# Kernel optimization log

Hardware: AMD Instinct MI355X
Metric: run time of the kernel (lower is better)

Reference implementation:

```python
import jax, jax.numpy as jnp
import numpy as np

B, S, D, H = 4, 2048, 1024, 16
HD = D // H
EPS = 1e-5

def _ln(x, g, b):
    mu = jnp.mean(x, axis=-1, keepdims=True)
    var = jnp.mean(jnp.square(x - mu), axis=-1, keepdims=True)
    return (x - mu) * jax.lax.rsqrt(var + EPS) * g + b

def setup_inputs() -> dict:
    key = jax.random.key(0)
    ks = jax.random.split(key, 6)
    W = 0.02  # GPT-2 style init scale keeps softmax unsaturated
    causal = jnp.tril(jnp.ones((S, S), dtype=bool))
    mask = jnp.where(causal, 0.0, -1e9).astype(jnp.float32)[None, None]
    return {
        "x": jax.random.normal(ks[0], (B, S, D), jnp.float32),
        "attention_mask": mask,
        "ln1_g": jnp.ones((D,), jnp.float32),
        "ln1_b": jnp.zeros((D,), jnp.float32),
        "w_qkv": jax.random.normal(ks[1], (D, 3 * D), jnp.float32) * W,
        "b_qkv": jnp.zeros((3 * D,), jnp.float32),
        "w_ao": jax.random.normal(ks[2], (D, D), jnp.float32) * W,
        "b_ao": jnp.zeros((D,), jnp.float32),
        "ln2_g": jnp.ones((D,), jnp.float32),
        "ln2_b": jnp.zeros((D,), jnp.float32),
        "w_fc": jax.random.normal(ks[3], (D, 4 * D), jnp.float32) * W,
        "b_fc": jnp.zeros((4 * D,), jnp.float32),
        "w_out": jax.random.normal(ks[4], (4 * D, D), jnp.float32) * W,
        "b_out": jnp.zeros((D,), jnp.float32),
    }

def reference(x, attention_mask, ln1_g, ln1_b, w_qkv, b_qkv, w_ao, b_ao,
              ln2_g, ln2_b, w_fc, b_fc, w_out, b_out):
    b, s, d = x.shape
    h = _ln(x, ln1_g, ln1_b)
    qkv = h @ w_qkv + b_qkv  # [B,S,3D]
    q, k, v = jnp.split(qkv, 3, axis=-1)
    def heads(t):  # [B,S,D] -> [B,H,S,HD]
        return t.reshape(b, s, H, HD).transpose(0, 2, 1, 3)
    q, k, v = heads(q), heads(k), heads(v)
    att = jnp.einsum('bhqd,bhkd->bhqk', q, k) / jnp.sqrt(jnp.float32(HD))
    att = att + attention_mask
    att = jax.nn.softmax(att, axis=-1)
    out = jnp.einsum('bhqk,bhkd->bhqd', att, v)
    out = out.transpose(0, 2, 1, 3).reshape(b, s, d)
    x = x + out @ w_ao + b_ao
    h2 = _ln(x, ln2_g, ln2_b)
    # torch nn.GELU() default is exact erf gelu
    mlp = jax.nn.gelu(h2 @ w_fc + b_fc, approximate=False) @ w_out + b_out
    return x + mlp
```

## Files before the change

kernel.cpp:

```cpp
#include <hip/hip_runtime.h>

typedef unsigned short u16;
typedef __attribute__((ext_vector_type(8))) short short8;
typedef __attribute__((ext_vector_type(4))) float floatx4;
typedef __attribute__((ext_vector_type(4))) unsigned short ushort4_t;

#define S_LEN 2048
#define DMODEL 1024
#define NHEAD 16
#define HDIM 64

__device__ __forceinline__ u16 f2bf(float f) {
    union { float f; unsigned u; } v; v.f = f;
    unsigned u = v.u;
    unsigned r = (u + 0x7fffu + ((u >> 16) & 1u)) >> 16;
    return (u16)r;
}

__device__ __forceinline__ u16 f2bf_fast(float f) {
    union { float f; unsigned u; } v; v.f = f;
    return (u16)((v.u + 0x8000u) >> 16);
}

__device__ __forceinline__ void gld_lds16(const u16* g, u16* l) {
    __builtin_amdgcn_global_load_lds((const __attribute__((address_space(1))) void*)g,
                                     (__attribute__((address_space(3))) void*)l,
                                     16, 0, 0);
}

__global__ __launch_bounds__(256) void ln_kernel(
    const float* __restrict__ x, const float* __restrict__ g,
    const float* __restrict__ b, u16* __restrict__ out)
{
    int row = blockIdx.x;
    int tid = threadIdx.x;
    const float4* xr = (const float4*)(x + (size_t)row * DMODEL);
    float4 v = xr[tid];
    float s  = v.x + v.y + v.z + v.w;
    float s2 = v.x * v.x + v.y * v.y + v.z * v.z + v.w * v.w;
    #pragma unroll
    for (int off = 1; off < 64; off <<= 1) {
        s  += __shfl_xor(s, off, 64);
        s2 += __shfl_xor(s2, off, 64);
    }
    __shared__ float red[2][4];
    int w = tid >> 6, lane = tid & 63;
    if (lane == 0) { red[0][w] = s; red[1][w] = s2; }
    __syncthreads();
    s  = red[0][0] + red[0][1] + red[0][2] + red[0][3];
    s2 = red[1][0] + red[1][1] + red[1][2] + red[1][3];
    float mu  = s * (1.0f / DMODEL);
    float var = s2 * (1.0f / DMODEL) - mu * mu;
    float inv = rsqrtf(var + 1e-5f);
    const float4* gr = (const float4*)g;
    const float4* br = (const float4*)b;
    float4 gv = gr[tid], bv = br[tid];
    u16* o = out + (size_t)row * DMODEL + tid * 4;
    o[0] = f2bf((v.x - mu) * inv * gv.x + bv.x);
    o[1] = f2bf((v.y - mu) * inv * gv.y + bv.y);
    o[2] = f2bf((v.z - mu) * inv * gv.z + bv.z);
    o[3] = f2bf((v.w - mu) * inv * gv.w + bv.w);
}

__global__ __launch_bounds__(256) void prep_kernel(
    const float* __restrict__ x, const float* __restrict__ g,
    const float* __restrict__ b, u16* __restrict__ out,
    const float* __restrict__ w0, u16* __restrict__ d0,
    const float* __restrict__ w1, u16* __restrict__ d1,
    const float* __restrict__ w2, u16* __restrict__ d2,
    const float* __restrict__ w3, u16* __restrict__ d3)
{
    int id = blockIdx.x;
    int tid = threadIdx.x;
    if (id < 8192) {
        int row = id;
        const float4* xr = (const float4*)(x + (size_t)row * DMODEL);
        float4 v = xr[tid];
        float s  = v.x + v.y + v.z + v.w;
        float s2 = v.x * v.x + v.y * v.y + v.z * v.z + v.w * v.w;
        #pragma unroll
        for (int off = 1; off < 64; off <<= 1) {
            s  += __shfl_xor(s, off, 64);
            s2 += __shfl_xor(s2, off, 64);
        }
        __shared__ float red[2][4];
        int w = tid >> 6, lane = tid & 63;
        if (lane == 0) { red[0][w] = s; red[1][w] = s2; }
        __syncthreads();
        s  = red[0][0] + red[0][1] + red[0][2] + red[0][3];
        s2 = red[1][0] + red[1][1] + red[1][2] + red[1][3];
        float mu  = s * (1.0f / DMODEL);
        float var = s2 * (1.0f / DMODEL) - mu * mu;
        float inv = rsqrtf(var + 1e-5f);
        const float4* gr = (const float4*)g;
        const float4* br = (const float4*)b;
        float4 gv = gr[tid], bv = br[tid];
        u16* o = out + (size_t)row * DMODEL + tid * 4;
        o[0] = f2bf((v.x - mu) * inv * gv.x + bv.x);
        o[1] = f2bf((v.y - mu) * inv * gv.y + bv.y);
        o[2] = f2bf((v.z - mu) * inv * gv.z + bv.z);
        o[3] = f2bf((v.w - mu) * inv * gv.w + bv.w);
        return;
    }
    id -= 8192;
    __shared__ float t[32][33];
    const float* w; u16* wt; int K, N, bx, by;
    if (id < 3072)      { w = w0; wt = d0; K = 1024; N = 3072; bx = id % 96;  by = id / 96;  }
    else if (id < 4096) { id -= 3072; w = w1; wt = d1; K = 1024; N = 1024; bx = id & 31;  by = id >> 5; }
    else if (id < 8192) { id -= 4096; w = w2; wt = d2; K = 1024; N = 4096; bx = id & 127; by = id >> 7; }
    else                { id -= 8192; w = w3; wt = d3; K = 4096; N = 1024; bx = id & 31;  by = id >> 5; }
    int n0 = bx * 32, k0 = by * 32;
    int xx = tid & 31, yy = tid >> 5;
    #pragma unroll
    for (int j = yy; j < 32; j += 8)
        t[j][xx] = w[(size_t)(k0 + j) * N + n0 + xx];
    __syncthreads();
    #pragma unroll
    for (int j = yy; j < 32; j += 8)
        wt[(size_t)(n0 + j) * K + k0 + xx] = f2bf(t[xx][j]);
}

template<int MODE>
__global__ __launch_bounds__(256) void gemm_bt(
    const u16* __restrict__ A, const u16* __restrict__ BT,
    int M, int N, int K,
    const float* __restrict__ bias, const float* __restrict__ res,
    float* __restrict__ fout,
    u16* __restrict__ o0, u16* __restrict__ o1, u16* __restrict__ o2)
{
    __shared__ __attribute__((aligned(16))) u16 As[2][128 * 64];
    __shared__ __attribute__((aligned(16))) u16 Bs[2][128 * 64];
    int tid = threadIdx.x;
    int lane = tid & 63, w = tid >> 6;
    int wm = (w >> 1) * 64, wn = (w & 1) * 64;
    int l15 = lane & 15, quad = lane >> 4;
    int rowBase = blockIdx.y * 128, colBase = blockIdx.x * 128;

    floatx4 acc[4][4] = {};

    const u16* pa[4];
    const u16* pbt[4];
    int scb[4];
    #pragma unroll
    for (int i = 0; i < 4; ++i) {
        int c  = i * 256 + tid;
        int r  = c >> 3;
        int cs = ((c & 7) ^ (r & 7)) * 8;
        pa[i]  = A  + (size_t)(rowBase + r) * K + cs;
        pbt[i] = BT + (size_t)(colBase + r) * K + cs;
        scb[i] = (i * 256 + (tid & 0xC0)) * 8;
    }

    int KT = K >> 6;

    #pragma unroll
    for (int i = 0; i < 4; ++i) {
        gld_lds16(pa[i],  &As[0][0] + scb[i]);
        gld_lds16(pbt[i], &Bs[0][0] + scb[i]);
    }

    for (int kt = 0; kt < KT; ++kt) {
        __syncthreads();

        if (kt + 1 < KT) {
            u16* abuf = &As[(kt + 1) & 1][0];
            u16* bbuf = &Bs[(kt + 1) & 1][0];
            #pragma unroll
            for (int i = 0; i < 4; ++i) {
                pa[i]  += 64;
                pbt[i] += 64;
                gld_lds16(pa[i],  abuf + scb[i]);
                gld_lds16(pbt[i], bbuf + scb[i]);
            }
        }

        const u16* as = &As[kt & 1][0];
        const u16* bs = &Bs[kt & 1][0];
        #pragma unroll
        for (int ks = 0; ks < 2; ++ks) {
            int sw = (((ks * 4 + quad) ^ (l15 & 7))) * 8;
            short8 af[4], bf[4];
            #pragma unroll
            for (int im = 0; im < 4; ++im)
                af[im] = *(const short8*)(as + (wm + im * 16 + l15) * 64 + sw);
            #pragma unroll
            for (int in = 0; in < 4; ++in)
                bf[in] = *(const short8*)(bs + (wn + in * 16 + l15) * 64 + sw);
            #pragma unroll
            for (int im = 0; im < 4; ++im)
                #pragma unroll
                for (int in = 0; in < 4; ++in)
                    acc[im][in] = __builtin_amdgcn_mfma_f32_16x16x32_bf16(af[im], bf[in], acc[im][in], 0, 0, 0);
        }
    }

    if (MODE == 0) {
        int t = colBase >> 10;
        int cb1023 = colBase & 1023;
        if (t == 2) {
            #pragma unroll
            for (int im = 0; im < 4; ++im) {
                int gr0 = rowBase + wm + im * 16 + quad * 4;
                int bb2 = gr0 >> 11, ss = gr0 & 2047;
                #pragma unroll
                for (int in = 0; in < 4; ++in) {
                    int gc = colBase + wn + in * 16 + l15;
                    int rr = cb1023 + wn + in * 16 + l15;
                    int hh = rr >> 6, hd = rr & 63;
                    float bv = bias[gc];
                    ushort4_t pk;
                    pk.x = f2bf_fast(acc[im][in][0] + bv);
                    pk.y = f2bf_fast(acc[im][in][1] + bv);
                    pk.z = f2bf_fast(acc[im][in][2] + bv);
                    pk.w = f2bf_fast(acc[im][in][3] + bv);
                    *(ushort4_t*)(o1 + ((size_t)(bb2 * NHEAD + hh) * HDIM + hd) * S_LEN + ss) = pk;
                }
            }
        } else {
            u16* qb = o0 + (size_t)t * 8388608;
            float sc = (t == 0) ? 0.125f : 1.0f;
            #pragma unroll
            for (int im = 0; im < 4; ++im) {
                #pragma unroll
                for (int in = 0; in < 4; ++in) {
                    #pragma unroll
                    for (int r = 0; r < 4; ++r) {
                        int gr = rowBase + wm + im * 16 + quad * 4 + r;
                        int gc = colBase + wn + in * 16 + l15;
                        float v = (acc[im][in][r] + bias[gc]) * sc;
                        int rr = cb1023 + wn + in * 16 + l15;
                        int hh = rr >> 6, hd = rr & 63;
                        int bb2 = gr >> 11, ss = gr & 2047;
                        qb[(((size_t)(bb2 * NHEAD + hh) * S_LEN + ss) * HDIM) + hd] = f2bf_fast(v);
                    }
                }
            }
        }
    } else {
        #pragma unroll
        for (int im = 0; im < 4; ++im) {
            #pragma unroll
            for (int in = 0; in < 4; ++in) {
                #pragma unroll
                for (int r = 0; r < 4; ++r) {
                    int gr = rowBase + wm + im * 16 + quad * 4 + r;
                    int gc = colBase + wn + in * 16 + l15;
                    float v = acc[im][in][r] + bias[gc];
                    if (MODE == 2) {
                        float p = v * (1.59576912f + 0.07135481f * v * v);
                        float e = __expf(-p);
                        float gl = v * __builtin_amdgcn_rcpf(1.0f + e);
                        o0[(size_t)gr * N + gc] = f2bf_fast(gl);
                    } else {
                        fout[(size_t)gr * N + gc] = v + res[(size_t)gr * N + gc];
                    }
                }
            }
        }
    }
}

template<int MODE>
__global__ __launch_bounds__(512, 2) void gemm256(
    const u16* __restrict__ A, const u16* __restrict__ BT,
    int M, int N, int K,
    const float* __restrict__ bias,
    u16* __restrict__ o0, u16* __restrict__ o1)
{
    __shared__ __attribute__((aligned(16))) u16 As[2][2][128 * 64];
    __shared__ __attribute__((aligned(16))) u16 Bs[2][2][128 * 64];
    int tid = threadIdx.x;
    int lane = tid & 63, w = tid >> 6;
    int wrow = w >> 2, wcol = w & 3;
    int l15 = lane & 15, quad = lane >> 4;
    int rowBase = blockIdx.y * 256, colBase = blockIdx.x * 256;
    int nrb = (wcol & 1) * 64;

    int swz[2] = { (quad ^ (l15 & 7)) * 8, ((4 + quad) ^ (l15 & 7)) * 8 };

    int cid0 = tid, cid1 = 512 + tid;
    int r0 = cid0 >> 3, r1 = cid1 >> 3;
    unsigned cs0 = (unsigned)(((cid0 & 7) ^ (r0 & 7)) * 8);
    unsigned cs1 = (unsigned)(((cid1 & 7) ^ (r1 & 7)) * 8);
    unsigned aoff0 = (unsigned)((rowBase + r0) * K) + cs0;
    unsigned aoff1 = (unsigned)((rowBase + r1) * K) + cs1;
    unsigned boff0 = (unsigned)((colBase + r0) * K) + cs0;
    unsigned boff1 = (unsigned)((colBase + r1) * K) + cs1;
    unsigned ldo0 = (unsigned)(cid0 * 8), ldo1 = (unsigned)(cid1 * 8);
    unsigned hK = (unsigned)(128 * K);

    floatx4 acc[8][4] = {};
    short8 af[4][2], bfL[2][2], bfH[2][2];

    int KT = K >> 6;

#define STG_A(db, tt, h) do { unsigned tb_ = (unsigned)(tt) * 64u + (h) * hK;      \
    gld_lds16(A + aoff0 + tb_, &As[db][h][0] + ldo0);                              \
    gld_lds16(A + aoff1 + tb_, &As[db][h][0] + ldo1); } while (0)
#define STG_B(db, tt, h) do { unsigned tb_ = (unsigned)(tt) * 64u + (h) * hK;      \
    gld_lds16(BT + boff0 + tb_, &Bs[db][h][0] + ldo0);                             \
    gld_lds16(BT + boff1 + tb_, &Bs[db][h][0] + ldo1); } while (0)
#define LDS_A(buf, MFB) do { const u16* ap_ = &As[buf][wrow][0];                   \
    _Pragma("unroll") for (int m_ = 0; m_ < 4; ++m_) {                             \
      af[m_][0] = *(const short8*)(ap_ + (((MFB) + m_) * 16 + l15) * 64 + swz[0]); \
      af[m_][1] = *(const short8*)(ap_ + (((MFB) + m_) * 16 + l15) * 64 + swz[1]); } } while (0)
#define LDS_B(buf, NFP, dst) do { const u16* bp_ = &Bs[buf][wcol >> 1][0];         \
    _Pragma("unroll") for (int n_ = 0; n_ < 2; ++n_) {                             \
      dst[n_][0] = *(const short8*)(bp_ + (nrb + ((NFP) * 2 + n_) * 16 + l15) * 64 + swz[0]); \
      dst[n_][1] = *(const short8*)(bp_ + (nrb + ((NFP) * 2 + n_) * 16 + l15) * 64 + swz[1]); } } while (0)
#define MFMA_Q(MFB, NFP, bsrc) do { __builtin_amdgcn_s_setprio(1);                 \
    _Pragma("unroll") for (int m_ = 0; m_ < 4; ++m_)                               \
    _Pragma("unroll") for (int n_ = 0; n_ < 2; ++n_) {                             \
      acc[(MFB) + m_][(NFP) * 2 + n_] = __builtin_amdgcn_mfma_f32_16x16x32_bf16(af[m_][0], bsrc[n_][0], acc[(MFB) + m_][(NFP) * 2 + n_], 0, 0, 0); \
      acc[(MFB) + m_][(NFP) * 2 + n_] = __builtin_amdgcn_mfma_f32_16x16x32_bf16(af[m_][1], bsrc[n_][1], acc[(MFB) + m_][(NFP) * 2 + n_], 0, 0, 0); } \
    __builtin_amdgcn_s_setprio(0); } while (0)
#define PH_MID() do { __builtin_amdgcn_sched_barrier(0);                           \
    __builtin_amdgcn_s_barrier();                                                  \
    asm volatile("s_waitcnt lgkmcnt(0)" ::: "memory");                             \
    __builtin_amdgcn_sched_barrier(0); } while (0)
#define PH_END() do { __builtin_amdgcn_sched_barrier(0);                           \
    __builtin_amdgcn_s_barrier(); } while (0)

    STG_A(0, 0, 0); STG_A(0, 0, 1);
    STG_B(0, 0, 0); STG_B(0, 0, 1);
    STG_B(1, 1, 0); STG_B(1, 1, 1);
    STG_A(1, 1, 0);
    asm volatile("s_waitcnt vmcnt(6)" ::: "memory");
    __builtin_amdgcn_s_barrier();

    for (int t = 0; t < KT; t += 2) {
        int t2 = (t + 2 < KT) ? t + 2 : KT - 1;
        int t3 = (t + 3 < KT) ? t + 3 : KT - 1;

        LDS_A(0, 0); LDS_B(0, 0, bfL);
        STG_A(1, t + 1, 1);
        asm volatile("s_waitcnt lgkmcnt(8)" ::: "memory");
        PH_MID(); MFMA_Q(0, 0, bfL); PH_END();

        LDS_B(0, 1, bfH);
        PH_MID(); MFMA_Q(0, 1, bfH); PH_END();

        LDS_A(0, 4);
        STG_B(0, t2, 0);
        PH_MID(); MFMA_Q(4, 1, bfH); PH_END();

        STG_B(0, t2, 1);
        STG_A(0, t2, 0);
        asm volatile("s_waitcnt vmcnt(6)" ::: "memory");
        PH_MID(); MFMA_Q(4, 0, bfL); PH_END();

        LDS_A(1, 0); LDS_B(1, 0, bfL);
        STG_A(0, t2, 1);
        asm volatile("s_waitcnt lgkmcnt(8)" ::: "memory");
        PH_MID(); MFMA_Q(0, 0, bfL); PH_END();

        LDS_B(1, 1, bfH);
        PH_MID(); MFMA_Q(0, 1, bfH); PH_END();

        LDS_A(1, 4);
        STG_B(1, t3, 0);
        PH_MID(); MFMA_Q(4, 1, bfH); PH_END();

        STG_B(1, t3, 1);
        STG_A(1, t3, 0);
        asm volatile("s_waitcnt vmcnt(6)" ::: "memory");
        PH_MID(); MFMA_Q(4, 0, bfL); PH_END();
    }
    asm volatile("s_waitcnt vmcnt(0)" ::: "memory");

#undef STG_A
#undef STG_B
#undef LDS_A
#undef LDS_B
#undef MFMA_Q
#undef PH_MID
#undef PH_END

    int wr0 = rowBase + wrow * 128 + quad * 4;
    int wc0 = colBase + wcol * 64 + l15;
    #pragma unroll
    for (int mf = 0; mf < 8; ++mf) {
        #pragma unroll
        for (int nf = 0; nf < 4; ++nf) {
            int gc = wc0 + nf * 16;
            float bv = bias[gc];
            #pragma unroll
            for (int r = 0; r < 4; ++r) {
                int gr = wr0 + mf * 16 + r;
                float v = acc[mf][nf][r] + bv;
                float p = v * (1.59576912f + 0.07135481f * v * v);
                float e = __expf(-p);
                float gl = v * __builtin_amdgcn_rcpf(1.0f + e);
                o0[(size_t)gr * N + gc] = f2bf_fast(gl);
            }
        }
    }
}

__global__ __launch_bounds__(256) void flash_attn(
    const u16* __restrict__ Q, const u16* __restrict__ Kb,
    const u16* __restrict__ Vt, u16* __restrict__ O)
{
    __shared__ __attribute__((aligned(16))) u16 Ks[2][64 * 64];
    __shared__ __attribute__((aligned(16))) u16 Vs[2][64 * 64];
    __shared__ __attribute__((aligned(16))) u16 Pl[4][2][16][64];
    int tid = threadIdx.x;
    int lane = tid & 63, w = tid >> 6;
    int l15 = lane & 15, quad = lane >> 4;
    int bh = blockIdx.x;
    int pp = blockIdx.y;
    int bb = bh >> 4, h = bh & 15;

    const u16* Kp0 = Kb + (size_t)bh * S_LEN * HDIM;
    const u16* Vp  = Vt + (size_t)bh * HDIM * S_LEN;

    int rstage = lane >> 3;
    int cstage = ((lane & 7) ^ rstage) * 8;
    int vrow0  = w * 8 + rstage;

    int ms[2] = {pp, 15 - pp};
    int pb = 0;

    #pragma unroll
    for (int i = 0; i < 2; ++i) {
        int row = i * 32 + vrow0;
        gld_lds16(Kp0 + row * HDIM + cstage, &Ks[0][0] + i * 2048 + w * 512);
        gld_lds16(Vp + (size_t)row * S_LEN + cstage, &Vs[0][0] + i * 2048 + w * 512);
    }

    #pragma unroll 1
    for (int sel = 0; sel < 2; ++sel) {
        int m = ms[sel];
        int q0 = m * 128;

        const u16* Qp = Q + ((size_t)bh * S_LEN + q0 + w * 16) * HDIM;
        short8 aq0[2], aq1[2];
        #pragma unroll
        for (int ks = 0; ks < 2; ++ks) {
            aq0[ks] = *(const short8*)(Qp + l15 * HDIM + ks * 32 + quad * 8);
            aq1[ks] = *(const short8*)(Qp + 64 * HDIM + l15 * HDIM + ks * 32 + quad * 8);
        }

        floatx4 acc_o0[4] = {}, acc_o1[4] = {};
        float rs0 = 0.f, rs1 = 0.f;

        int KT = 2 * m + 2;

        auto softmax_store = [&](floatx4 (&sa)[4], float& rs, int st, bool diag) {
            #pragma unroll
            for (int nt = 0; nt < 4; ++nt) {
                ushort4_t pk;
                #pragma unroll
                for (int r = 0; r < 4; ++r) {
                    float sv = sa[nt][r];
                    if (diag) {
                        int kc = nt * 16 + quad * 4 + r;
                        if (kc > w * 16 + l15) sv = -1e30f;
                    }
                    float pv = __expf(sv);
                    rs += pv;
                    pk[r] = f2bf_fast(pv);
                }
                int chSw = (nt * 4 + quad) ^ (l15 & 14);
                *(ushort4_t*)(&Pl[w][st][l15][chSw * 4]) = pk;
            }
        };

        #pragma unroll 1
        for (int kt = 0; kt < KT; ++kt) {
            __syncthreads();
            int cur = pb;

            int nk = (kt + 1 < KT) ? (kt + 1) : ((sel < 1) ? 0 : -1);
            if (nk >= 0) {
                pb ^= 1;
                const u16* Kg = Kp0 + (size_t)nk * 64 * HDIM;
                const u16* Vg = Vp + nk * 64;
                u16* kb_ = &Ks[pb][0];
                u16* vb_ = &Vs[pb][0];
                #pragma unroll
                for (int i = 0; i < 2; ++i) {
                    int row = i * 32 + vrow0;
                    gld_lds16(Kg + row * HDIM + cstage, kb_ + i * 2048 + w * 512);
                    gld_lds16(Vg + (size_t)row * S_LEN + cstage, vb_ + i * 2048 + w * 512);
                }
            }

            const u16* kcur = &Ks[cur][0];
            const u16* vcur = &Vs[cur][0];

            bool a0 = (kt < KT - 1);

            floatx4 s0a[4] = {}, s1a[4] = {};
            __builtin_amdgcn_s_setprio(1);
            #pragma unroll
            for (int nt = 0; nt < 4; ++nt) {
                #pragma unroll
                for (int ks = 0; ks < 2; ++ks) {
                    int sw = ((ks * 4 + quad) ^ (l15 & 7)) * 8;
                    short8 bk = *(const short8*)(kcur + (nt * 16 + l15) * 64 + sw);
                    s0a[nt] = __builtin_amdgcn_mfma_f32_16x16x32_bf16(bk, aq0[ks], s0a[nt], 0, 0, 0);
                    s1a[nt] = __builtin_amdgcn_mfma_f32_16x16x32_bf16(bk, aq1[ks], s1a[nt], 0, 0, 0);
                }
            }
            __builtin_amdgcn_s_setprio(0);

            if (a0) softmax_store(s0a, rs0, 0, kt == KT - 2);
            softmax_store(s1a, rs1, 1, kt == KT - 1);

            short8 pf0[2] = {}, pf1[2];
            if (a0) {
                #pragma unroll
                for (int ks = 0; ks < 2; ++ks) {
                    int pc = ((ks * 8 + quad * 2) ^ (l15 & 14)) * 4;
                    pf0[ks] = *(const short8*)(&Pl[w][0][l15][pc]);
                }
            }
            #pragma unroll
            for (int ks = 0; ks < 2; ++ks) {
                int pc = ((ks * 8 + quad * 2) ^ (l15 & 14)) * 4;
                pf1[ks] = *(const short8*)(&Pl[w][1][l15][pc]);
            }

            __builtin_amdgcn_s_setprio(1);
            #pragma unroll
            for (int nt = 0; nt < 4; ++nt) {
                #pragma unroll
                for (int ks = 0; ks < 2; ++ks) {
                    int sw = ((ks * 4 + quad) ^ (l15 & 7)) * 8;
                    short8 bv = *(const short8*)(vcur + (nt * 16 + l15) * 64 + sw);
                    acc_o0[nt] = __builtin_amdgcn_mfma_f32_16x16x32_bf16(pf0[ks], bv, acc_o0[nt], 0, 0, 0);
                    acc_o1[nt] = __builtin_amdgcn_mfma_f32_16x16x32_bf16(pf1[ks], bv, acc_o1[nt], 0, 0, 0);
                }
            }
            __builtin_amdgcn_s_setprio(0);
        }

        rs0 += __shfl_xor(rs0, 16, 64);
        rs0 += __shfl_xor(rs0, 32, 64);
        rs1 += __shfl_xor(rs1, 16, 64);
        rs1 += __shfl_xor(rs1, 32, 64);
        float inv0 = 1.0f / rs0;
        float inv1 = 1.0f / rs1;

        float iv0[4], iv1[4];
        #pragma unroll
        for (int r = 0; r < 4; ++r) {
            iv0[r] = __shfl(inv0, quad * 4 + r, 64);
            iv1[r] = __shfl(inv1, quad * 4 + r, 64);
        }

        #pragma unroll
        for (int nt = 0; nt < 4; ++nt) {
            #pragma unroll
            for (int r = 0; r < 4; ++r) {
                int qr = q0 + w * 16 + quad * 4 + r;
                int hd = nt * 16 + l15;
                O[((size_t)bb * S_LEN + qr) * DMODEL + h * HDIM + hd] = f2bf(acc_o0[nt][r] * iv0[r]);
                O[((size_t)bb * S_LEN + qr + 64) * DMODEL + h * HDIM + hd] = f2bf(acc_o1[nt][r] * iv1[r]);
            }
        }
    }
}

extern "C" void kernel_launch(void* const* d_in, const int* in_sizes, int n_in,
                              void* d_out, int out_size, void* d_ws, size_t ws_size,
                              hipStream_t stream)
{
    const float* x    = (const float*)d_in[0];
    const float* ln1g = (const float*)d_in[2];
    const float* ln1b = (const float*)d_in[3];
    const float* wqkv = (const float*)d_in[4];
    const float* bqkv = (const float*)d_in[5];
    const float* wao  = (const float*)d_in[6];
    const float* bao  = (const float*)d_in[7];
    const float* ln2g = (const float*)d_in[8];
    const float* ln2b = (const float*)d_in[9];
    const float* wfc  = (const float*)d_in[10];
    const float* bfc  = (const float*)d_in[11];
    const float* wout = (const float*)d_in[12];
    const float* bout = (const float*)d_in[13];
    float* out = (float*)d_out;

    char* ws = (char*)d_ws;
    u16* wqkvT = (u16*)(ws + 0);
    u16* waoT  = (u16*)(ws + 6291456);
    u16* wfcT  = (u16*)(ws + 8388608);
    u16* woutT = (u16*)(ws + 16777216);
    u16* hb    = (u16*)(ws + 25165824);
    u16* QKVb  = (u16*)(ws + 41943040);
    u16* Vtb   = (u16*)(ws + 92274688);
    u16* Gb    = (u16*)(ws + 41943040);

    u16* Qb   = QKVb;
    u16* Kbuf = QKVb + 8388608;

    prep_kernel<<<dim3(20480), 256, 0, stream>>>(
        x, ln1g, ln1b, hb,
        wqkv, wqkvT, wao, waoT, wfc, wfcT, wout, woutT);

    gemm_bt<0><<<dim3(3072/128, 8192/128), 256, 0, stream>>>(
        hb, wqkvT, 8192, 3072, 1024, bqkv, nullptr, nullptr, QKVb, Vtb, nullptr);

    flash_attn<<<dim3(64, 8), 256, 0, stream>>>(Qb, Kbuf, Vtb, hb);

    gemm_bt<1><<<dim3(1024/128, 8192/128), 256, 0, stream>>>(
        hb, waoT, 8192, 1024, 1024, bao, x, out, nullptr, nullptr, nullptr);

    ln_kernel<<<8192, 256, 0, stream>>>(out, ln2g, ln2b, hb);

    gemm256<2><<<dim3(4096/256, 8192/256), 512, 0, stream>>>(
        hb, wfcT, 8192, 4096, 1024, bfc, Gb, nullptr);

    gemm_bt<3><<<dim3(1024/128, 8192/128), 256, 0, stream>>>(
        Gb, woutT, 8192, 1024, 4096, bout, out, out, nullptr, nullptr, nullptr);
}
```

Measured before the change: 480.2 us.

## Keep softmax probabilities in registers by permuting V transpose key order

The flash attention kernel no longer stages the softmax probability tile through shared memory. Each lane packs its S-accumulator outputs straight into the MFMA A-operand registers. To make that register layout line up with the PV multiply, the QKV GEMM epilogue now writes the transposed V with a bit permutation of the sequence index inside each 64-key block, so the K dimension ordering matches. This removes an LDS write/read round trip per tile and frees shared memory, but it couples the V layout to the MFMA register mapping.

```diff
diff --git a/kernel.cpp b/kernel.cpp
--- a/kernel.cpp
+++ b/kernel.cpp
@@ -202,6 +202,11 @@
             for (int im = 0; im < 4; ++im) {
                 int gr0 = rowBase + wm + im * 16 + quad * 4;
                 int bb2 = gr0 >> 11, ss = gr0 & 2047;
+                int sl = ss & 63;
+                int ssg = (ss & ~63) | (sl & 35)
+                        | (((sl >> 3) & 1) << 4)
+                        | (((sl >> 2) & 1) << 3)
+                        | (((sl >> 4) & 1) << 2);
                 #pragma unroll
                 for (int in = 0; in < 4; ++in) {
                     int gc = colBase + wn + in * 16 + l15;
@@ -213,7 +218,7 @@
                     pk.y = f2bf_fast(acc[im][in][1] + bv);
                     pk.z = f2bf_fast(acc[im][in][2] + bv);
                     pk.w = f2bf_fast(acc[im][in][3] + bv);
-                    *(ushort4_t*)(o1 + ((size_t)(bb2 * NHEAD + hh) * HDIM + hd) * S_LEN + ss) = pk;
+                    *(ushort4_t*)(o1 + ((size_t)(bb2 * NHEAD + hh) * HDIM + hd) * S_LEN + ssg) = pk;
                 }
             }
         } else {
@@ -403,7 +408,6 @@
 {
     __shared__ __attribute__((aligned(16))) u16 Ks[2][64 * 64];
     __shared__ __attribute__((aligned(16))) u16 Vs[2][64 * 64];
-    __shared__ __attribute__((aligned(16))) u16 Pl[4][2][16][64];
     int tid = threadIdx.x;
     int lane = tid & 63, w = tid >> 6;
     int l15 = lane & 15, quad = lane >> 4;
@@ -446,10 +450,10 @@
 
         int KT = 2 * m + 2;
 
-        auto softmax_store = [&](floatx4 (&sa)[4], float& rs, int st, bool diag) {
+        auto softmax_pack = [&](floatx4 (&sa)[4], float& rs, unsigned (&pA)[4][2], bool diag) {
             #pragma unroll
             for (int nt = 0; nt < 4; ++nt) {
-                ushort4_t pk;
+                u16 pk[4];
                 #pragma unroll
                 for (int r = 0; r < 4; ++r) {
                     float sv = sa[nt][r];
@@ -461,8 +465,8 @@
                     rs += pv;
                     pk[r] = f2bf_fast(pv);
                 }
-                int chSw = (nt * 4 + quad) ^ (l15 & 14);
-                *(ushort4_t*)(&Pl[w][st][l15][chSw * 4]) = pk;
+                pA[nt][0] = (unsigned)pk[0] | ((unsigned)pk[1] << 16);
+                pA[nt][1] = (unsigned)pk[2] | ((unsigned)pk[3] << 16);
             }
         };
 
@@ -505,21 +509,22 @@
             }
             __builtin_amdgcn_s_setprio(0);
 
-            if (a0) softmax_store(s0a, rs0, 0, kt == KT - 2);
-            softmax_store(s1a, rs1, 1, kt == KT - 1);
+            unsigned pA0[4][2], pA1[4][2];
+            if (a0) softmax_pack(s0a, rs0, pA0, kt == KT - 2);
+            softmax_pack(s1a, rs1, pA1, kt == KT - 1);
 
             short8 pf0[2] = {}, pf1[2];
-            if (a0) {
-                #pragma unroll
-                for (int ks = 0; ks < 2; ++ks) {
-                    int pc = ((ks * 8 + quad * 2) ^ (l15 & 14)) * 4;
-                    pf0[ks] = *(const short8*)(&Pl[w][0][l15][pc]);
-                }
-            }
             #pragma unroll
             for (int ks = 0; ks < 2; ++ks) {
-                int pc = ((ks * 8 + quad * 2) ^ (l15 & 14)) * 4;
-                pf1[ks] = *(const short8*)(&Pl[w][1][l15][pc]);
+                union { unsigned u[4]; short8 s; } c0, c1;
+                if (a0) {
+                    c0.u[0] = pA0[2 * ks][0]; c0.u[1] = pA0[2 * ks][1];
+                    c0.u[2] = pA0[2 * ks + 1][0]; c0.u[3] = pA0[2 * ks + 1][1];
+                    pf0[ks] = c0.s;
+                }
+                c1.u[0] = pA1[2 * ks][0]; c1.u[1] = pA1[2 * ks][1];
+                c1.u[2] = pA1[2 * ks + 1][0]; c1.u[3] = pA1[2 * ks + 1][1];
+                pf1[ks] = c1.s;
             }
 
             __builtin_amdgcn_s_setprio(1);
```

Result: no change. 476.7 us (-0.7%).
